# Optimization experiments

Measured on AMD Instinct MI355X. Metric: run time of the kernel, lower is better.

The kernel has to match this reference:

```python
import jax, jax.numpy as jnp
import numpy as np

E, M, IN, OUT = 8, 8192, 2048, 8192


def setup_inputs() -> dict:
    key = jax.random.key(0)
    k1, k2, k3 = jax.random.split(key, 3)
    inputs = jax.random.normal(k1, (M, IN), dtype=jnp.float32)
    # truncated_normal(-3,3) scaled by init_scale/sqrt(In), matching MoELinear.init
    weight = jax.random.truncated_normal(k2, -3.0, 3.0, (E, IN, OUT), dtype=jnp.float32) * (1.0 / np.sqrt(IN))
    bias = jax.random.normal(k3, (OUT,), dtype=jnp.float32) * 0.02
    # tokens are pre-sorted by expert; balanced routing: M/E tokens per expert
    group_sizes = jnp.full((E,), M // E, dtype=jnp.int32)
    return {"inputs": inputs, "weight": weight, "group_sizes": group_sizes, "bias": bias}


def _ragged_matmul(inputs, weight, group_sizes):
    """Grouped GEMM: out[m] = inputs[m] @ weight[expert_of(m)].

    Tokens are contiguous per expert; group_sizes[e] gives the count for
    expert e. Same math as jax.lax.ragged_dot / megablox gmm.
    """
    n_experts = weight.shape[0]
    m = inputs.shape[0]
    # static-length repeat -> per-token expert id, jit-safe
    expert_ids = jnp.repeat(jnp.arange(n_experts, dtype=group_sizes.dtype),
                            group_sizes, total_repeat_length=m)  # [M]

    def body(acc, ew):
        e, w = ew  # w: [In, Out]
        mask = (expert_ids == e).astype(inputs.dtype)  # [M]
        return acc + (inputs * mask[:, None]) @ w, None

    acc0 = jnp.zeros((m, weight.shape[2]), dtype=inputs.dtype)
    out, _ = jax.lax.scan(body, acc0, (jnp.arange(n_experts, dtype=group_sizes.dtype), weight))
    return out


def reference(inputs, weight, group_sizes, bias):
    # MoELinear.__call__ (ragged_dot path): grouped matmul + bias
    return _ragged_matmul(inputs, weight, group_sizes) + bias
```

## Files before the change

kernel.cpp:

```cpp
#include <hip/hip_runtime.h>
#include <stdint.h>

#define E_ 8
#define M_ 8192
#define K_ 2048
#define N_ 8192

#define BM 256
#define BN 256
#define BK 64
#define NT (K_ / BK)
#define LDS_BYTES 131072

typedef __attribute__((ext_vector_type(8))) short bf16x8;
typedef __attribute__((ext_vector_type(4))) float f32x4;
typedef __attribute__((ext_vector_type(8))) unsigned short us8;

__device__ __forceinline__ unsigned short f2bf(float f) {
  union { float f; uint32_t u; } v; v.f = f;
  uint32_t u = v.u;
  uint32_t r = (u + 0x7FFFu + ((u >> 16) & 1u)) >> 16;
  return (unsigned short)r;
}

__device__ __forceinline__ void gload_lds16(const void* g, void* l) {
  __builtin_amdgcn_global_load_lds(
      (const __attribute__((address_space(1))) unsigned int*)g,
      (__attribute__((address_space(3))) unsigned int*)l,
      16, 0, 0);
}

__global__ __launch_bounds__(256) void conv_a(const float* __restrict__ A,
                                              unsigned short* __restrict__ Ab,
                                              int n8) {
  int stride = gridDim.x * blockDim.x;
  for (int idx = blockIdx.x * blockDim.x + threadIdx.x; idx < n8; idx += stride) {
    const float4* p = reinterpret_cast<const float4*>(A) + (size_t)idx * 2;
    float4 x0 = p[0], x1 = p[1];
    us8 o;
    o[0] = f2bf(x0.x); o[1] = f2bf(x0.y); o[2] = f2bf(x0.z); o[3] = f2bf(x0.w);
    o[4] = f2bf(x1.x); o[5] = f2bf(x1.y); o[6] = f2bf(x1.z); o[7] = f2bf(x1.w);
    *reinterpret_cast<us8*>(Ab + (size_t)idx * 8) = o;
  }
}

__global__ __launch_bounds__(256) void conv_wT(const float* __restrict__ W,
                                               unsigned short* __restrict__ Wt,
                                               int e_fixed) {
  __shared__ float t[64][65];
  int tid = threadIdx.x;
  int tx = tid & 63, ty = tid >> 6;
  int n0 = blockIdx.x * 64, k0 = blockIdx.y * 64;
  int e = (gridDim.z > 1) ? blockIdx.z : e_fixed;
  size_t win = (size_t)e * K_ * N_;
  size_t wout = (gridDim.z > 1) ? win : 0;

  #pragma unroll
  for (int r = 0; r < 16; ++r) {
    int kl = r * 4 + ty;
    t[kl][tx] = W[win + (size_t)(k0 + kl) * N_ + n0 + tx];
  }
  __syncthreads();
  int px = tid & 31, py = tid >> 5;
  #pragma unroll
  for (int r = 0; r < 8; ++r) {
    int nl = r * 8 + py;
    unsigned int pack = (unsigned int)f2bf(t[2 * px][nl]) |
                        ((unsigned int)f2bf(t[2 * px + 1][nl]) << 16);
    *reinterpret_cast<unsigned int*>(Wt + wout + (size_t)(n0 + nl) * K_ + k0 + 2 * px) = pack;
  }
}

__global__ __launch_bounds__(512, 2) void moe_gemm_bf16(
    const unsigned short* __restrict__ Ab,
    const unsigned short* __restrict__ Wt,
    const int* __restrict__ gs,
    const float* __restrict__ bias,
    float* __restrict__ C,
    int only_expert, size_t wt_stride) {
  extern __shared__ char smem[];

  int tile_n = blockIdx.x;
  int tile_m = blockIdx.y;

  int expert = -1, row_start = 0, rows = 0;
  if (only_expert >= 0) {
    int off = 0;
    for (int e = 0; e < only_expert; ++e) off += gs[e];
    int g = gs[only_expert];
    int t0 = tile_m * BM;
    if (t0 >= g) return;
    expert = only_expert;
    row_start = off + t0;
    rows = min(BM, g - t0);
  } else {
    int acc = 0, off = 0;
    for (int e = 0; e < E_; ++e) {
      int g = gs[e];
      int t = (g + BM - 1) / BM;
      if (expert < 0 && tile_m < acc + t) {
        int lt = tile_m - acc;
        expert = e;
        row_start = off + lt * BM;
        rows = min(BM, g - lt * BM);
      }
      acc += t;
      off += g;
    }
    if (expert < 0) return;
  }

  const unsigned short* WtE = Wt + (size_t)expert * wt_stride;

  int tid = threadIdx.x;
  int lane = tid & 63;
  int wave = tid >> 6;
  int wr = wave >> 2;
  int wc = wave & 3;
  int bh = wc >> 1;
  int ln15 = lane & 15;
  int n0 = tile_n * BN;

  int slot0 = (((lane >> 4) ^ (ln15 & 7)) << 4);
  int aBase = wr * 16384 + ln15 * 128;
  int bBase = 32768 + bh * 16384 + (wc & 1) * 8192 + ln15 * 128;

  int soff = tid * 16;
  int crow = tid >> 3;
  int lslot = (tid & 7) ^ (crow & 7);
  int scol = lslot * 8;

  const unsigned short* aS[4];
  const unsigned short* bS[4];
  #pragma unroll
  for (int c = 0; c < 4; ++c) {
    int r = c * 64 + crow;
    int gr = r < rows ? r : 0;
    aS[c] = Ab + (size_t)(row_start + gr) * K_ + scol;
    bS[c] = WtE + (size_t)(n0 + r) * K_ + scol;
  }

#define STG_A(DB, c, kt) \
  gload_lds16(aS[c] + (kt) * 64, smem + (DB) + (c) * 8192 + soff)
#define STG_B(DB, c, kt) \
  gload_lds16(bS[c] + (kt) * 64, smem + (DB) + 32768 + (c) * 8192 + soff)

  f32x4 acc4[8][4];
  #pragma unroll
  for (int i = 0; i < 8; ++i)
    #pragma unroll
    for (int j = 0; j < 4; ++j)
      acc4[i][j] = f32x4{0.f, 0.f, 0.f, 0.f};

#define DS_A(frag, DB, MH, KS)                                                \
  _Pragma("unroll") for (int mi = 0; mi < 4; ++mi)                            \
    frag[mi] = *(const bf16x8*)(smem + (DB) + aBase + (MH) * 8192 +           \
                                mi * 2048 + (slot0 ^ ((KS) << 6)));
#define DS_B(frag, DB, KS)                                                    \
  _Pragma("unroll") for (int nj = 0; nj < 4; ++nj)                            \
    frag[nj] = *(const bf16x8*)(smem + (DB) + bBase + nj * 2048 +             \
                                (slot0 ^ ((KS) << 6)));
#define MFMA16(MB, af, bf)                                                    \
  __builtin_amdgcn_s_setprio(1);                                              \
  _Pragma("unroll") for (int mi = 0; mi < 4; ++mi)                            \
    _Pragma("unroll") for (int nj = 0; nj < 4; ++nj)                          \
      acc4[(MB) + mi][nj] = __builtin_amdgcn_mfma_f32_16x16x32_bf16(          \
          af[mi], bf[nj], acc4[(MB) + mi][nj], 0, 0, 0);                      \
  __builtin_amdgcn_s_setprio(0);

#define TILE4(DB, DBN, KTN)                                                   \
  do {                                                                        \
    bf16x8 af[4], bf[4];                                                      \
                                                                      \
    DS_A(af, DB, 0, 0); DS_B(bf, DB, 0);                                      \
    STG_B(DBN, 0, KTN); STG_B(DBN, 1, KTN);                                   \
    __builtin_amdgcn_s_barrier();                                             \
    asm volatile("s_waitcnt lgkmcnt(0)" ::: "memory");                        \
    __builtin_amdgcn_sched_barrier(0);                                        \
    MFMA16(0, af, bf);                                                        \
    asm volatile("s_waitcnt vmcnt(2)" ::: "memory");                          \
    __builtin_amdgcn_s_barrier();                                             \
                                                   \
    DS_A(af, DB, 1, 0);                                                       \
    STG_B(DBN, 2, KTN); STG_B(DBN, 3, KTN);                                   \
    __builtin_amdgcn_s_barrier();                                             \
    asm volatile("s_waitcnt lgkmcnt(0)" ::: "memory");                        \
    __builtin_amdgcn_sched_barrier(0);                                        \
    MFMA16(4, af, bf);                                                        \
    __builtin_amdgcn_s_barrier();                                             \
                                                                      \
    DS_A(af, DB, 0, 1); DS_B(bf, DB, 1);                                      \
    STG_A(DBN, 0, KTN); STG_A(DBN, 2, KTN);                                   \
    __builtin_amdgcn_s_barrier();                                             \
    asm volatile("s_waitcnt lgkmcnt(0)" ::: "memory");                        \
    __builtin_amdgcn_sched_barrier(0);                                        \
    MFMA16(0, af, bf);                                                        \
    __builtin_amdgcn_s_barrier();                                             \
                                                                      \
    DS_A(af, DB, 1, 1);                                                       \
    STG_A(DBN, 1, KTN); STG_A(DBN, 3, KTN);                                   \
    __builtin_amdgcn_s_barrier();                                             \
    asm volatile("s_waitcnt lgkmcnt(0)" ::: "memory");                        \
    __builtin_amdgcn_sched_barrier(0);                                        \
    MFMA16(4, af, bf);                                                        \
    asm volatile("s_waitcnt vmcnt(2)" ::: "memory");                          \
    __builtin_amdgcn_s_barrier();                                             \
  } while (0)

  STG_B(0, 0, 0); STG_B(0, 1, 0); STG_B(0, 2, 0); STG_B(0, 3, 0);
  STG_A(0, 0, 0); STG_A(0, 2, 0);
  STG_A(0, 1, 0); STG_A(0, 3, 0);
  asm volatile("s_waitcnt vmcnt(2)" ::: "memory");
  __builtin_amdgcn_s_barrier();

  for (int t2 = 0; t2 < NT; t2 += 2) {
    int k2 = (t2 + 2 >= NT) ? 0 : t2 + 2;
    TILE4(0, 65536, t2 + 1);
    TILE4(65536, 0, k2);
  }
#undef TILE4
#undef DS_A
#undef DS_B
#undef MFMA16
#undef STG_A
#undef STG_B

  asm volatile("s_waitcnt vmcnt(0)" ::: "memory");

  float bv[4];
  #pragma unroll
  for (int nj = 0; nj < 4; ++nj) bv[nj] = bias[n0 + wc * 64 + nj * 16 + ln15];
  #pragma unroll
  for (int mi = 0; mi < 8; ++mi) {
    int r0 = wr * 128 + mi * 16 + (lane >> 4) * 4;
    #pragma unroll
    for (int r = 0; r < 4; ++r) {
      int lr = r0 + r;
      if (lr < rows) {
        float* Cp = C + (size_t)(row_start + lr) * N_ + n0 + wc * 64 + ln15;
        #pragma unroll
        for (int nj = 0; nj < 4; ++nj) Cp[nj * 16] = acc4[mi][nj][r] + bv[nj];
      }
    }
  }
}

__global__ __launch_bounds__(256) void moe_naive(const float* __restrict__ A,
                                                 const float* __restrict__ W,
                                                 const int* __restrict__ gs,
                                                 const float* __restrict__ bias,
                                                 float* __restrict__ C) {
  int col = blockIdx.x * 16 + (threadIdx.x & 15);
  int row = blockIdx.y * 16 + (threadIdx.x >> 4);
  int acc = 0, e = E_ - 1;
  for (int i = 0; i < E_; ++i) {
    int g = gs[i];
    if (row >= acc && row < acc + g) { e = i; break; }
    acc += g;
  }
  const float* a = A + (size_t)row * K_;
  const float* w = W + (size_t)e * K_ * N_ + col;
  float s = 0.f;
  for (int k = 0; k < K_; ++k) s += a[k] * w[(size_t)k * N_];
  C[(size_t)row * N_ + col] = s + bias[col];
}

extern "C" void kernel_launch(void* const* d_in, const int* in_sizes, int n_in,
                              void* d_out, int out_size, void* d_ws, size_t ws_size,
                              hipStream_t stream) {
  const float* A = (const float*)d_in[0];
  const float* W = (const float*)d_in[1];
  const int* gs = (const int*)d_in[2];
  const float* bias = (const float*)d_in[3];
  float* C = (float*)d_out;

  const size_t needA = (size_t)M_ * K_ * 2;
  const size_t needWall = (size_t)E_ * K_ * N_ * 2;
  const size_t needW1 = (size_t)K_ * N_ * 2;

  (void)hipFuncSetAttribute((const void*)moe_gemm_bf16,
                            hipFuncAttributeMaxDynamicSharedMemorySize, LDS_BYTES);

  if (ws_size >= needA + needWall) {
    unsigned short* Abf = (unsigned short*)d_ws;
    unsigned short* Wtb = (unsigned short*)((char*)d_ws + needA);
    conv_a<<<2048, 256, 0, stream>>>(A, Abf, (M_ * K_) / 8);
    dim3 gw(N_ / 64, K_ / 64, E_);
    conv_wT<<<gw, 256, 0, stream>>>(W, Wtb, 0);
    dim3 gg(N_ / BN, M_ / BM + E_);
    moe_gemm_bf16<<<gg, 512, LDS_BYTES, stream>>>(Abf, Wtb, gs, bias, C, -1, (size_t)N_ * K_);
  } else if (ws_size >= needA + needW1) {
    unsigned short* Abf = (unsigned short*)d_ws;
    unsigned short* Wtb = (unsigned short*)((char*)d_ws + needA);
    conv_a<<<2048, 256, 0, stream>>>(A, Abf, (M_ * K_) / 8);
    for (int e = 0; e < E_; ++e) {
      dim3 gw(N_ / 64, K_ / 64, 1);
      conv_wT<<<gw, 256, 0, stream>>>(W, Wtb, e);
      dim3 gg(N_ / BN, M_ / BM);
      moe_gemm_bf16<<<gg, 512, LDS_BYTES, stream>>>(Abf, Wtb, gs, bias, C, e, 0);
    }
  } else {
    dim3 gn(N_ / 16, M_ / 16);
    moe_naive<<<gn, 256, 0, stream>>>(A, W, gs, bias, C);
  }
}
```

Before: 428.3 us.

## Fuse weight fp32-to-bf16 conversion and transpose into the grouped GEMM main loop

Removes the separate conv_wT pass that converted and transposed all expert weights into a bf16 workspace. The GEMM now loads fp32 weights straight from global memory into registers, converts them to bf16 and writes them into swizzled LDS inside the pipelined loop. A staging loads are reordered and the LDS swizzle changes to match. This saves a full read and write of the 512 MB weight tensor, but each weight tile is now converted once per M-tile (32 times), which doubles global weight traffic per tile and adds conversion ALU work and register pressure in the loop.

```diff
diff --git a/kernel.cpp b/kernel.cpp
--- a/kernel.cpp
+++ b/kernel.cpp
@@ -1,4 +1,5 @@
 #include <hip/hip_runtime.h>
+#include <hip/hip_bf16.h>
 #include <stdint.h>
 
 #define E_ 8
@@ -21,6 +22,12 @@
   uint32_t u = v.u;
   uint32_t r = (u + 0x7FFFu + ((u >> 16) & 1u)) >> 16;
   return (unsigned short)r;
+}
+
+__device__ __forceinline__ unsigned short f2bf_hw(float f) {
+  union { __hip_bfloat16 h; unsigned short u; } v;
+  v.h = __float2bfloat16(f);
+  return v.u;
 }
 
 __device__ __forceinline__ void gload_lds16(const void* g, void* l) {
@@ -44,56 +51,19 @@
   }
 }
 
-__global__ __launch_bounds__(256) void conv_wT(const float* __restrict__ W,
-                                               unsigned short* __restrict__ Wt,
-                                               int e_fixed) {
-  __shared__ float t[64][65];
-  int tid = threadIdx.x;
-  int tx = tid & 63, ty = tid >> 6;
-  int n0 = blockIdx.x * 64, k0 = blockIdx.y * 64;
-  int e = (gridDim.z > 1) ? blockIdx.z : e_fixed;
-  size_t win = (size_t)e * K_ * N_;
-  size_t wout = (gridDim.z > 1) ? win : 0;
-
-  #pragma unroll
-  for (int r = 0; r < 16; ++r) {
-    int kl = r * 4 + ty;
-    t[kl][tx] = W[win + (size_t)(k0 + kl) * N_ + n0 + tx];
-  }
-  __syncthreads();
-  int px = tid & 31, py = tid >> 5;
-  #pragma unroll
-  for (int r = 0; r < 8; ++r) {
-    int nl = r * 8 + py;
-    unsigned int pack = (unsigned int)f2bf(t[2 * px][nl]) |
-                        ((unsigned int)f2bf(t[2 * px + 1][nl]) << 16);
-    *reinterpret_cast<unsigned int*>(Wt + wout + (size_t)(n0 + nl) * K_ + k0 + 2 * px) = pack;
-  }
-}
-
-__global__ __launch_bounds__(512, 2) void moe_gemm_bf16(
+__global__ __launch_bounds__(512, 2) void moe_gemm_fused(
     const unsigned short* __restrict__ Ab,
-    const unsigned short* __restrict__ Wt,
+    const float* __restrict__ W,
     const int* __restrict__ gs,
     const float* __restrict__ bias,
-    float* __restrict__ C,
-    int only_expert, size_t wt_stride) {
+    float* __restrict__ C) {
   extern __shared__ char smem[];
 
   int tile_n = blockIdx.x;
   int tile_m = blockIdx.y;
 
   int expert = -1, row_start = 0, rows = 0;
-  if (only_expert >= 0) {
-    int off = 0;
-    for (int e = 0; e < only_expert; ++e) off += gs[e];
-    int g = gs[only_expert];
-    int t0 = tile_m * BM;
-    if (t0 >= g) return;
-    expert = only_expert;
-    row_start = off + t0;
-    rows = min(BM, g - t0);
-  } else {
+  {
     int acc = 0, off = 0;
     for (int e = 0; e < E_; ++e) {
       int g = gs[e];
@@ -110,7 +80,7 @@
     if (expert < 0) return;
   }
 
-  const unsigned short* WtE = Wt + (size_t)expert * wt_stride;
+  const float* WfE = W + (size_t)expert * K_ * N_;
 
   int tid = threadIdx.x;
   int lane = tid & 63;
@@ -121,29 +91,50 @@
   int ln15 = lane & 15;
   int n0 = tile_n * BN;
 
-  int slot0 = (((lane >> 4) ^ (ln15 & 7)) << 4);
+  int slot0 = (((lane >> 4) ^ ((ln15 >> 1) & 7)) << 4);
   int aBase = wr * 16384 + ln15 * 128;
   int bBase = 32768 + bh * 16384 + (wc & 1) * 8192 + ln15 * 128;
 
   int soff = tid * 16;
   int crow = tid >> 3;
-  int lslot = (tid & 7) ^ (crow & 7);
-  int scol = lslot * 8;
-
+  int lslot = (tid & 7) ^ ((crow >> 1) & 7);
+  int scolA = lslot * 8;
   const unsigned short* aS[4];
-  const unsigned short* bS[4];
   #pragma unroll
   for (int c = 0; c < 4; ++c) {
     int r = c * 64 + crow;
     int gr = r < rows ? r : 0;
-    aS[c] = Ab + (size_t)(row_start + gr) * K_ + scol;
-    bS[c] = WtE + (size_t)(n0 + r) * K_ + scol;
-  }
-
+    aS[c] = Ab + (size_t)(row_start + gr) * K_ + scolA;
+  }
 #define STG_A(DB, c, kt) \
   gload_lds16(aS[c] + (kt) * 64, smem + (DB) + (c) * 8192 + soff)
-#define STG_B(DB, c, kt) \
-  gload_lds16(bS[c] + (kt) * 64, smem + (DB) + 32768 + (c) * 8192 + soff)
+
+  int nB = (tid & 127) * 2;
+  int kb0 = tid >> 7;
+  const float* wB = WfE + (size_t)(n0 + nB);
+  int sB0 = (kb0 ^ ((nB >> 1) & 7)) << 4;
+  int sB1 = ((kb0 + 4) ^ ((nB >> 1) & 7)) << 4;
+  int bw00 = 32768 + nB * 128 + sB0;
+  int bw01 = 32768 + (nB + 1) * 128 + sB0;
+  int bw10 = 32768 + nB * 128 + sB1;
+  int bw11 = 32768 + (nB + 1) * 128 + sB1;
+
+  float2 fB0[8], fB1[8];
+
+#define LOAD_B(arr, KB, KT)                                                   \
+  _Pragma("unroll") for (int j = 0; j < 8; ++j)                               \
+    arr[j] = *(const float2*)(wB + (size_t)((KT) * 64 + (KB) * 8 + j) * N_);
+
+#define CVT_WRITE(arr, WE, WO, DBN)                                           \
+  do {                                                                        \
+    us8 oe, oo;                                                               \
+    _Pragma("unroll") for (int p = 0; p < 8; ++p) {                           \
+      oe[p] = f2bf_hw(arr[p].x);                                              \
+      oo[p] = f2bf_hw(arr[p].y);                                              \
+    }                                                                         \
+    *(us8*)(smem + (DBN) + (WE)) = oe;                                        \
+    *(us8*)(smem + (DBN) + (WO)) = oo;                                        \
+  } while (0)
 
   f32x4 acc4[8][4];
   #pragma unroll
@@ -173,16 +164,19 @@
     bf16x8 af[4], bf[4];                                                      \
                                                                       \
     DS_A(af, DB, 0, 0); DS_B(bf, DB, 0);                                      \
-    STG_B(DBN, 0, KTN); STG_B(DBN, 1, KTN);                                   \
+    LOAD_B(fB0, kb0, KTN);                                                    \
+    __builtin_amdgcn_sched_barrier(0);                                        \
     __builtin_amdgcn_s_barrier();                                             \
     asm volatile("s_waitcnt lgkmcnt(0)" ::: "memory");                        \
     __builtin_amdgcn_sched_barrier(0);                                        \
     MFMA16(0, af, bf);                                                        \
-    asm volatile("s_waitcnt vmcnt(2)" ::: "memory");                          \
-    __builtin_amdgcn_s_barrier();                                             \
-                                                   \
+    __builtin_amdgcn_s_barrier();                                             \
+                                              \
     DS_A(af, DB, 1, 0);                                                       \
-    STG_B(DBN, 2, KTN); STG_B(DBN, 3, KTN);                                   \
+    LOAD_B(fB1, kb0 + 4, KTN);                                                \
+    STG_A(DBN, 0, KTN); STG_A(DBN, 1, KTN);                                   \
+    STG_A(DBN, 2, KTN); STG_A(DBN, 3, KTN);                                   \
+    __builtin_amdgcn_sched_barrier(0);                                        \
     __builtin_amdgcn_s_barrier();                                             \
     asm volatile("s_waitcnt lgkmcnt(0)" ::: "memory");                        \
     __builtin_amdgcn_sched_barrier(0);                                        \
@@ -190,7 +184,7 @@
     __builtin_amdgcn_s_barrier();                                             \
                                                                       \
     DS_A(af, DB, 0, 1); DS_B(bf, DB, 1);                                      \
-    STG_A(DBN, 0, KTN); STG_A(DBN, 2, KTN);                                   \
+    CVT_WRITE(fB0, bw00, bw01, DBN);                                          \
     __builtin_amdgcn_s_barrier();                                             \
     asm volatile("s_waitcnt lgkmcnt(0)" ::: "memory");                        \
     __builtin_amdgcn_sched_barrier(0);                                        \
@@ -198,19 +192,22 @@
     __builtin_amdgcn_s_barrier();                                             \
                                                                       \
     DS_A(af, DB, 1, 1);                                                       \
-    STG_A(DBN, 1, KTN); STG_A(DBN, 3, KTN);                                   \
+    CVT_WRITE(fB1, bw10, bw11, DBN);                                          \
     __builtin_amdgcn_s_barrier();                                             \
     asm volatile("s_waitcnt lgkmcnt(0)" ::: "memory");                        \
     __builtin_amdgcn_sched_barrier(0);                                        \
     MFMA16(4, af, bf);                                                        \
-    asm volatile("s_waitcnt vmcnt(2)" ::: "memory");                          \
+    asm volatile("s_waitcnt vmcnt(0)" ::: "memory");  \
     __builtin_amdgcn_s_barrier();                                             \
   } while (0)
 
-  STG_B(0, 0, 0); STG_B(0, 1, 0); STG_B(0, 2, 0); STG_B(0, 3, 0);
-  STG_A(0, 0, 0); STG_A(0, 2, 0);
-  STG_A(0, 1, 0); STG_A(0, 3, 0);
-  asm volatile("s_waitcnt vmcnt(2)" ::: "memory");
+  LOAD_B(fB0, kb0, 0);
+  LOAD_B(fB1, kb0 + 4, 0);
+  STG_A(0, 0, 0); STG_A(0, 1, 0); STG_A(0, 2, 0); STG_A(0, 3, 0);
+  CVT_WRITE(fB0, bw00, bw01, 0);
+  CVT_WRITE(fB1, bw10, bw11, 0);
+  asm volatile("s_waitcnt vmcnt(0)" ::: "memory");
+  asm volatile("s_waitcnt lgkmcnt(0)" ::: "memory");
   __builtin_amdgcn_s_barrier();
 
   for (int t2 = 0; t2 < NT; t2 += 2) {
@@ -223,9 +220,8 @@
 #undef DS_B
 #undef MFMA16
 #undef STG_A
-#undef STG_B
-
-  asm volatile("s_waitcnt vmcnt(0)" ::: "memory");
+#undef LOAD_B
+#undef CVT_WRITE
 
   float bv[4];
   #pragma unroll
@@ -275,30 +271,15 @@
   float* C = (float*)d_out;
 
   const size_t needA = (size_t)M_ * K_ * 2;
-  const size_t needWall = (size_t)E_ * K_ * N_ * 2;
-  const size_t needW1 = (size_t)K_ * N_ * 2;
-
-  (void)hipFuncSetAttribute((const void*)moe_gemm_bf16,
+
+  (void)hipFuncSetAttribute((const void*)moe_gemm_fused,
                             hipFuncAttributeMaxDynamicSharedMemorySize, LDS_BYTES);
 
-  if (ws_size >= needA + needWall) {
+  if (ws_size >= needA) {
     unsigned short* Abf = (unsigned short*)d_ws;
-    unsigned short* Wtb = (unsigned short*)((char*)d_ws + needA);
     conv_a<<<2048, 256, 0, stream>>>(A, Abf, (M_ * K_) / 8);
-    dim3 gw(N_ / 64, K_ / 64, E_);
-    conv_wT<<<gw, 256, 0, stream>>>(W, Wtb, 0);
     dim3 gg(N_ / BN, M_ / BM + E_);
-    moe_gemm_bf16<<<gg, 512, LDS_BYTES, stream>>>(Abf, Wtb, gs, bias, C, -1, (size_t)N_ * K_);
-  } else if (ws_size >= needA + needW1) {
-    unsigned short* Abf = (unsigned short*)d_ws;
-    unsigned short* Wtb = (unsigned short*)((char*)d_ws + needA);
-    conv_a<<<2048, 256, 0, stream>>>(A, Abf, (M_ * K_) / 8);
-    for (int e = 0; e < E_; ++e) {
-      dim3 gw(N_ / 64, K_ / 64, 1);
-      conv_wT<<<gw, 256, 0, stream>>>(W, Wtb, e);
-      dim3 gg(N_ / BN, M_ / BM);
-      moe_gemm_bf16<<<gg, 512, LDS_BYTES, stream>>>(Abf, Wtb, gs, bias, C, e, 0);
-    }
+    moe_gemm_fused<<<gg, 512, LDS_BYTES, stream>>>(Abf, W, gs, bias, C);
   } else {
     dim3 gn(N_ / 16, M_ / 16);
     moe_naive<<<gn, 256, 0, stream>>>(A, W, gs, bias, C);
```

After: 441.0 us. 3.0% more time.

## Switch grouped GEMM inner loop from 16x16x32 to 32x32x16 MFMA

Applied to the files above, without the earlier changes.

Replaces the 16x16x32 bf16 MFMA tiling with 32x32x16 MFMA instructions. Each wave now holds 4x2 accumulators of 16 floats instead of 8x4 of 4 floats. LDS fragment reads, swizzle addressing and the epilogue store mapping are reworked to match the 32-lane row layout. The goal is fewer LDS reads per FLOP and higher MFMA throughput per instruction, at the risk of new LDS bank conflicts from the changed swizzle and a less coalesced output store pattern.

```diff
diff --git a/kernel.cpp b/kernel.cpp
--- a/kernel.cpp
+++ b/kernel.cpp
@@ -13,7 +13,7 @@
 #define LDS_BYTES 131072
 
 typedef __attribute__((ext_vector_type(8))) short bf16x8;
-typedef __attribute__((ext_vector_type(4))) float f32x4;
+typedef __attribute__((ext_vector_type(16))) float f32x16;
 typedef __attribute__((ext_vector_type(8))) unsigned short us8;
 
 __device__ __forceinline__ unsigned short f2bf(float f) {
@@ -118,12 +118,13 @@
   int wr = wave >> 2;
   int wc = wave & 3;
   int bh = wc >> 1;
-  int ln15 = lane & 15;
+  int ln31 = lane & 31;
+  int l5 = lane >> 5;
   int n0 = tile_n * BN;
 
-  int slot0 = (((lane >> 4) ^ (ln15 & 7)) << 4);
-  int aBase = wr * 16384 + ln15 * 128;
-  int bBase = 32768 + bh * 16384 + (wc & 1) * 8192 + ln15 * 128;
+  int slot032 = ((l5 ^ (lane & 7)) << 4);
+  int aBase = wr * 16384 + ln31 * 128;
+  int bBase = 32768 + (bh * 128 + (wc & 1) * 64 + ln31) * 128;
 
   int soff = tid * 16;
   int crow = tid >> 3;
@@ -145,64 +146,68 @@
 #define STG_B(DB, c, kt) \
   gload_lds16(bS[c] + (kt) * 64, smem + (DB) + 32768 + (c) * 8192 + soff)
 
-  f32x4 acc4[8][4];
-  #pragma unroll
-  for (int i = 0; i < 8; ++i)
+  f32x16 acc4[4][2];
+  #pragma unroll
+  for (int i = 0; i < 4; ++i)
     #pragma unroll
-    for (int j = 0; j < 4; ++j)
-      acc4[i][j] = f32x4{0.f, 0.f, 0.f, 0.f};
-
-#define DS_A(frag, DB, MH, KS)                                                \
-  _Pragma("unroll") for (int mi = 0; mi < 4; ++mi)                            \
-    frag[mi] = *(const bf16x8*)(smem + (DB) + aBase + (MH) * 8192 +           \
-                                mi * 2048 + (slot0 ^ ((KS) << 6)));
-#define DS_B(frag, DB, KS)                                                    \
-  _Pragma("unroll") for (int nj = 0; nj < 4; ++nj)                            \
-    frag[nj] = *(const bf16x8*)(smem + (DB) + bBase + nj * 2048 +             \
-                                (slot0 ^ ((KS) << 6)));
-#define MFMA16(MB, af, bf)                                                    \
+    for (int j = 0; j < 2; ++j)
+      #pragma unroll
+      for (int r = 0; r < 16; ++r) acc4[i][j][r] = 0.f;
+
+#define DS_A2(frag, DB, KK, MIB)                                              \
+  _Pragma("unroll") for (int m = 0; m < 2; ++m)                               \
+    _Pragma("unroll") for (int ks = 0; ks < 2; ++ks)                          \
+      frag[m][ks] = *(const bf16x8*)(smem + (DB) + aBase + ((MIB) + m) * 4096 \
+                                     + (slot032 ^ (ks << 5) ^ ((KK) << 6)));
+#define DS_B2(frag, DB, KK)                                                   \
+  _Pragma("unroll") for (int nj = 0; nj < 2; ++nj)                            \
+    _Pragma("unroll") for (int ks = 0; ks < 2; ++ks)                          \
+      frag[nj][ks] = *(const bf16x8*)(smem + (DB) + bBase + nj * 4096         \
+                                      + (slot032 ^ (ks << 5) ^ ((KK) << 6)));
+#define MFMA8(MIB, afr, bfr)                                                  \
   __builtin_amdgcn_s_setprio(1);                                              \
-  _Pragma("unroll") for (int mi = 0; mi < 4; ++mi)                            \
-    _Pragma("unroll") for (int nj = 0; nj < 4; ++nj)                          \
-      acc4[(MB) + mi][nj] = __builtin_amdgcn_mfma_f32_16x16x32_bf16(          \
-          af[mi], bf[nj], acc4[(MB) + mi][nj], 0, 0, 0);                      \
+  _Pragma("unroll") for (int ks = 0; ks < 2; ++ks)                            \
+    _Pragma("unroll") for (int m = 0; m < 2; ++m)                             \
+      _Pragma("unroll") for (int nj = 0; nj < 2; ++nj)                        \
+        acc4[(MIB) + m][nj] = __builtin_amdgcn_mfma_f32_32x32x16_bf16(        \
+            afr[m][ks], bfr[nj][ks], acc4[(MIB) + m][nj], 0, 0, 0);           \
   __builtin_amdgcn_s_setprio(0);
 
 #define TILE4(DB, DBN, KTN)                                                   \
   do {                                                                        \
-    bf16x8 af[4], bf[4];                                                      \
+    bf16x8 af[2][2], bf[2][2];                                                \
                                                                       \
-    DS_A(af, DB, 0, 0); DS_B(bf, DB, 0);                                      \
+    DS_A2(af, DB, 0, 0); DS_B2(bf, DB, 0);                                    \
     STG_B(DBN, 0, KTN); STG_B(DBN, 1, KTN);                                   \
     __builtin_amdgcn_s_barrier();                                             \
     asm volatile("s_waitcnt lgkmcnt(0)" ::: "memory");                        \
     __builtin_amdgcn_sched_barrier(0);                                        \
-    MFMA16(0, af, bf);                                                        \
+    MFMA8(0, af, bf);                                                         \
     asm volatile("s_waitcnt vmcnt(2)" ::: "memory");                          \
     __builtin_amdgcn_s_barrier();                                             \
                                                    \
-    DS_A(af, DB, 1, 0);                                                       \
+    DS_A2(af, DB, 0, 2);                                                      \
     STG_B(DBN, 2, KTN); STG_B(DBN, 3, KTN);                                   \
     __builtin_amdgcn_s_barrier();                                             \
     asm volatile("s_waitcnt lgkmcnt(0)" ::: "memory");                        \
     __builtin_amdgcn_sched_barrier(0);                                        \
-    MFMA16(4, af, bf);                                                        \
+    MFMA8(2, af, bf);                                                         \
     __builtin_amdgcn_s_barrier();                                             \
                                                                       \
-    DS_A(af, DB, 0, 1); DS_B(bf, DB, 1);                                      \
+    DS_A2(af, DB, 1, 0); DS_B2(bf, DB, 1);                                    \
     STG_A(DBN, 0, KTN); STG_A(DBN, 2, KTN);                                   \
     __builtin_amdgcn_s_barrier();                                             \
     asm volatile("s_waitcnt lgkmcnt(0)" ::: "memory");                        \
     __builtin_amdgcn_sched_barrier(0);                                        \
-    MFMA16(0, af, bf);                                                        \
+    MFMA8(0, af, bf);                                                         \
     __builtin_amdgcn_s_barrier();                                             \
                                                                       \
-    DS_A(af, DB, 1, 1);                                                       \
+    DS_A2(af, DB, 1, 2);                                                      \
     STG_A(DBN, 1, KTN); STG_A(DBN, 3, KTN);                                   \
     __builtin_amdgcn_s_barrier();                                             \
     asm volatile("s_waitcnt lgkmcnt(0)" ::: "memory");                        \
     __builtin_amdgcn_sched_barrier(0);                                        \
-    MFMA16(4, af, bf);                                                        \
+    MFMA8(2, af, bf);                                                         \
     asm volatile("s_waitcnt vmcnt(2)" ::: "memory");                          \
     __builtin_amdgcn_s_barrier();                                             \
   } while (0)
@@ -219,27 +224,30 @@
     TILE4(65536, 0, k2);
   }
 #undef TILE4
-#undef DS_A
-#undef DS_B
-#undef MFMA16
+#undef DS_A2
+#undef DS_B2
+#undef MFMA8
 #undef STG_A
 #undef STG_B
 
   asm volatile("s_waitcnt vmcnt(0)" ::: "memory");
 
-  float bv[4];
-  #pragma unroll
-  for (int nj = 0; nj < 4; ++nj) bv[nj] = bias[n0 + wc * 64 + nj * 16 + ln15];
-  #pragma unroll
-  for (int mi = 0; mi < 8; ++mi) {
-    int r0 = wr * 128 + mi * 16 + (lane >> 4) * 4;
+  float bv[2];
+  #pragma unroll
+  for (int nj = 0; nj < 2; ++nj) bv[nj] = bias[n0 + wc * 64 + nj * 32 + ln31];
+  #pragma unroll
+  for (int mi = 0; mi < 4; ++mi) {
     #pragma unroll
-    for (int r = 0; r < 4; ++r) {
-      int lr = r0 + r;
-      if (lr < rows) {
-        float* Cp = C + (size_t)(row_start + lr) * N_ + n0 + wc * 64 + ln15;
-        #pragma unroll
-        for (int nj = 0; nj < 4; ++nj) Cp[nj * 16] = acc4[mi][nj][r] + bv[nj];
+    for (int g = 0; g < 4; ++g) {
+      #pragma unroll
+      for (int rb = 0; rb < 4; ++rb) {
+        int reg = g * 4 + rb;
+        int lr = wr * 128 + mi * 32 + rb + g * 8 + l5 * 4;
+        if (lr < rows) {
+          float* Cp = C + (size_t)(row_start + lr) * N_ + n0 + wc * 64 + ln31;
+          #pragma unroll
+          for (int nj = 0; nj < 2; ++nj) Cp[nj * 32] = acc4[mi][nj][reg] + bv[nj];
+        }
       }
     }
   }
```

Result: slower. 460.7 us (+7.6%).
